# Kernel tuning notes

Hardware: AMD Instinct MI355X
Metric: run time of the kernel (lower is better)

## Reference

```python
import jax, jax.numpy as jnp
import numpy as np
from jax import lax

V, E, H = 32000, 512, 1024  # vocab, embedding_dim, hidden_dim
S, B, T = 50, 64, 10        # src len, batch, max decode steps
SOS = 0


def setup_inputs() -> dict:
    key = jax.random.key(0)
    ks = jax.random.split(key, 16)
    sc = 0.02
    n = jax.random.normal
    return {
        "enc_out": n(ks[0], (S, B, 2 * H), jnp.float32),
        "hidden": n(ks[1], (1, B, H), jnp.float32),
        "target": jax.random.randint(ks[2], (B, T), 0, V),
        "emb": n(ks[3], (V, E), jnp.float32) * sc,
        "w_ih": n(ks[4], (3 * H, E), jnp.float32) * sc,
        "w_hh": n(ks[5], (3 * H, H), jnp.float32) * sc,
        "b_ih": n(ks[6], (3 * H,), jnp.float32) * sc,
        "b_hh": n(ks[7], (3 * H,), jnp.float32) * sc,
        "wa_w": n(ks[8], (H, H), jnp.float32) * sc,
        "wa_b": n(ks[9], (H,), jnp.float32) * sc,
        "ua_w": n(ks[10], (H, 2 * H), jnp.float32) * sc,
        "ua_b": n(ks[11], (H,), jnp.float32) * sc,
        "va_w": n(ks[12], (1, H), jnp.float32) * sc,
        "va_b": n(ks[13], (1,), jnp.float32) * sc,
    }


def reference(enc_out, hidden, target, emb, w_ih, w_hh, b_ih, b_hh,
              wa_w, wa_b, ua_w, ua_b, va_w, va_b):
    b, t = target.shape

    def gru_cell(x, h):
        gi = x @ w_ih.T + b_ih          # [B, 3H]
        gh = h @ w_hh.T + b_hh          # [B, 3H]
        ir, iz, inn = jnp.split(gi, 3, axis=-1)
        hr, hz, hn = jnp.split(gh, 3, axis=-1)
        r = jax.nn.sigmoid(ir + hr)
        z = jax.nn.sigmoid(iz + hz)
        nng = jnp.tanh(inn + r * hn)
        return (1.0 - z) * nng + z * h

    # teacher-forced decoder inputs: [SOS, target[:, :-1]] -> [T, B]
    dec_in = jnp.concatenate(
        [jnp.full((b, 1), SOS, dtype=target.dtype), target[:, : t - 1]], axis=1)
    xs = emb[dec_in].transpose(1, 0, 2)  # [T, B, E] (dropout is identity in eval)

    def step(h, x):
        h2 = gru_cell(x, h)
        return h2, h2

    h_last, hs = lax.scan(step, hidden[0], xs)   # hs: [T, B, H]

    keys = enc_out.transpose(1, 0, 2)            # [B, S, 2H]
    uk = keys @ ua_w.T + ua_b                    # [B, S, H]
    wq = hs @ wa_w.T + wa_b                      # [T, B, H]
    # additive (Bahdanau) scores: [T, B, S]
    scores = (jnp.tanh(wq[:, :, None, :] + uk[None]) @ va_w.T + va_b)[..., 0]
    weights = jax.nn.softmax(scores, axis=-1)    # over source positions
    context = jnp.einsum('tbs,bsd->btd', weights, keys)  # [B, T, 2H]
    out = jax.nn.log_softmax(context, axis=-1)   # [B, T, 2H]
    return out, h_last
```

## Files before the change

### kernel.cpp

```cpp
#include <hip/hip_runtime.h>
#include <math.h>

#define VOCAB 32000
#define E_DIM 512
#define H_DIM 1024
#define S_LEN 50
#define B_SZ 64
#define T_LEN 10
#define H3 (3 * H_DIM)
#define D2H (2 * H_DIM)

typedef __attribute__((ext_vector_type(8))) short short8;
typedef __attribute__((ext_vector_type(4))) float floatx4;

__device__ __forceinline__ ushort f2b(float f) {
    union { float f; uint32_t u; } x; x.f = f;
    uint32_t r = (x.u + 0x7fff + ((x.u >> 16) & 1)) >> 16;
    return (ushort)r;
}
__device__ __forceinline__ float b2f(ushort u) {
    union { float f; uint32_t u; } x; x.u = ((uint32_t)u) << 16;
    return x.f;
}
__device__ __forceinline__ float fast_sigmoid(float x) {
    x = fminf(fmaxf(x, -30.f), 30.f);
    return 1.f / (1.f + __expf(-x));
}
__device__ __forceinline__ float fast_tanh(float x) {
    x = fminf(fmaxf(x, -15.f), 15.f);
    float e = __expf(2.f * x);
    return (e - 1.f) / (e + 1.f);
}

#define PB0 1536
#define PB1 (PB0 + 3072)
#define PB2 (PB1 + 2048)
#define PB3 (PB2 + 1024)
#define PB4 (PB3 + 3200)
#define PB5 (PB4 + 640)
#define PB6 (PB5 + 64)

__device__ __forceinline__ void cvt_chunk(const float* src, ushort* dst, int i) {
    float4 v = ((const float4*)src)[i];
    ushort4 o;
    o.x = f2b(v.x); o.y = f2b(v.y); o.z = f2b(v.z); o.w = f2b(v.w);
    ((ushort4*)dst)[i] = o;
}

__global__ __launch_bounds__(256) void prep(
    const float* __restrict__ w_ih, ushort* __restrict__ w_ihb,
    const float* __restrict__ w_hh, ushort* __restrict__ w_hhb,
    const float* __restrict__ ua_w, ushort* __restrict__ ua_wb,
    const float* __restrict__ wa_w, ushort* __restrict__ wa_wb,
    const float* __restrict__ enc_out, ushort* __restrict__ keysb,
    const int* __restrict__ target, const float* __restrict__ emb,
    ushort* __restrict__ Xb,
    const float* __restrict__ hidden, ushort* __restrict__ hb0,
    int* __restrict__ bar) {
    int bid = blockIdx.x, tid = threadIdx.x;
    if (bid == 0) {
        for (int i = tid; i < 4096; i += 256)
            __hip_atomic_store(&bar[i], 0, __ATOMIC_RELAXED, __HIP_MEMORY_SCOPE_SYSTEM);
    }
    if (bid < PB0) {
        cvt_chunk(w_ih, w_ihb, bid * 256 + tid);
    } else if (bid < PB1) {
        cvt_chunk(w_hh, w_hhb, (bid - PB0) * 256 + tid);
    } else if (bid < PB2) {
        cvt_chunk(ua_w, ua_wb, (bid - PB1) * 256 + tid);
    } else if (bid < PB3) {
        cvt_chunk(wa_w, wa_wb, (bid - PB2) * 256 + tid);
    } else if (bid < PB4) {
        int bs = bid - PB3;
        int b = bs / S_LEN, s = bs % S_LEN;
        const float* src = enc_out + ((size_t)s * B_SZ + b) * D2H;
        ushort* dst = keysb + (size_t)bs * D2H;
#pragma unroll
        for (int p = 0; p < 2; ++p) {
            int i = tid + p * 256;
            float4 v = ((const float4*)src)[i];
            ushort4 o;
            o.x = f2b(v.x); o.y = f2b(v.y); o.z = f2b(v.z); o.w = f2b(v.w);
            ((ushort4*)dst)[i] = o;
        }
    } else if (bid < PB5) {
        int m = bid - PB4;
        int t = m / B_SZ, b = m % B_SZ;
        int idx = (t == 0) ? 0 : target[b * T_LEN + (t - 1)];
        if (tid < 128) {
            const float* src = emb + (size_t)idx * E_DIM;
            float4 v = ((const float4*)src)[tid];
            ushort4 o;
            o.x = f2b(v.x); o.y = f2b(v.y); o.z = f2b(v.z); o.w = f2b(v.w);
            ((ushort4*)(Xb + (size_t)m * E_DIM))[tid] = o;
        }
    } else {
        cvt_chunk(hidden, hb0, (bid - PB5) * 256 + tid);
    }
}

struct GemmArgs {
    const ushort* A; const ushort* W; const float* bias;
    float* Cf; ushort* C16;
    int M, N, K, nbn, nblk;
};

__global__ __launch_bounds__(256) void gemm_bf16(GemmArgs g0, GemmArgs g1) {
    const bool first = (int)blockIdx.x < g0.nblk;
    GemmArgs g = first ? g0 : g1;
    const int bid = first ? blockIdx.x : (blockIdx.x - g0.nblk);

    __shared__ ushort As[64 * 72];
    __shared__ ushort Bs[128 * 72];

    const int tid = threadIdx.x;
    const int w = tid >> 6, lane = tid & 63;
    const int lm = lane & 15, q = lane >> 4;
    const int wm = w >> 1, wn = w & 1;
    const int n0 = (bid % g.nbn) * 128;
    const int m0 = (bid / g.nbn) * 64;
    const int K = g.K;

    floatx4 acc[2][4];
#pragma unroll
    for (int i = 0; i < 2; ++i)
#pragma unroll
        for (int j = 0; j < 4; ++j)
            acc[i][j] = (floatx4){0.f, 0.f, 0.f, 0.f};

    short8 ar[2], br[4];
    auto load_tiles = [&](int k0) {
#pragma unroll
        for (int p = 0; p < 2; ++p) {
            int c = tid + p * 256;
            ar[p] = *(const short8*)&g.A[(size_t)(m0 + (c >> 3)) * K + k0 + (c & 7) * 8];
        }
#pragma unroll
        for (int p = 0; p < 4; ++p) {
            int c = tid + p * 256;
            br[p] = *(const short8*)&g.W[(size_t)(n0 + (c >> 3)) * K + k0 + (c & 7) * 8];
        }
    };

    load_tiles(0);
    for (int k0 = 0; k0 < K; k0 += 64) {
#pragma unroll
        for (int p = 0; p < 2; ++p) {
            int c = tid + p * 256;
            *(short8*)&As[(c >> 3) * 72 + (c & 7) * 8] = ar[p];
        }
#pragma unroll
        for (int p = 0; p < 4; ++p) {
            int c = tid + p * 256;
            *(short8*)&Bs[(c >> 3) * 72 + (c & 7) * 8] = br[p];
        }
        __syncthreads();
        if (k0 + 64 < K) load_tiles(k0 + 64);

#pragma unroll
        for (int kk = 0; kk < 2; ++kk) {
            short8 af[2], bf[4];
#pragma unroll
            for (int i = 0; i < 2; ++i)
                af[i] = *(const short8*)&As[(wm * 32 + i * 16 + lm) * 72 + kk * 32 + q * 8];
#pragma unroll
            for (int j = 0; j < 4; ++j)
                bf[j] = *(const short8*)&Bs[(wn * 64 + j * 16 + lm) * 72 + kk * 32 + q * 8];
#pragma unroll
            for (int i = 0; i < 2; ++i)
#pragma unroll
                for (int j = 0; j < 4; ++j)
                    acc[i][j] = __builtin_amdgcn_mfma_f32_16x16x32_bf16(af[i], bf[j], acc[i][j], 0, 0, 0);
        }
        __syncthreads();
    }

    float bv[4];
#pragma unroll
    for (int j = 0; j < 4; ++j)
        bv[j] = g.bias[n0 + wn * 64 + j * 16 + lm];
#pragma unroll
    for (int i = 0; i < 2; ++i) {
#pragma unroll
        for (int j = 0; j < 4; ++j) {
            int col = n0 + wn * 64 + j * 16 + lm;
#pragma unroll
            for (int r = 0; r < 4; ++r) {
                int row = m0 + wm * 32 + i * 16 + q * 4 + r;
                float v = acc[i][j][r] + bv[j];
                if (g.C16) g.C16[(size_t)row * g.N + col] = f2b(v);
                else       g.Cf[(size_t)row * g.N + col] = v;
            }
        }
    }
}

#define GRU_BLOCKS 64
#define WS_STRIDE 1032

__device__ __forceinline__ void grid_barrier(int* __restrict__ bar, int t, int bid) {
    __syncthreads();
    if (threadIdx.x == 0) {
        int g = bid & 7;
        int sub = __hip_atomic_fetch_add(&bar[(t * 8 + g) * 32], 1,
                                         __ATOMIC_RELAXED, __HIP_MEMORY_SCOPE_SYSTEM);
        if (sub == 7) {
            int m = __hip_atomic_fetch_add(&bar[2560 + t * 32], 1,
                                           __ATOMIC_RELAXED, __HIP_MEMORY_SCOPE_SYSTEM);
            if (m == 7)
                __hip_atomic_store(&bar[3040], t + 1,
                                   __ATOMIC_RELAXED, __HIP_MEMORY_SCOPE_SYSTEM);
        }
        while (__hip_atomic_load(&bar[3040], __ATOMIC_RELAXED,
                                 __HIP_MEMORY_SCOPE_SYSTEM) <= t)
            __builtin_amdgcn_s_sleep(1);
    }
    __syncthreads();
}

__global__ __launch_bounds__(256, 1) void gru_persistent(
    const ushort* __restrict__ w_hhb, const float* __restrict__ bhh,
    const float* __restrict__ GI, const float* __restrict__ hidden,
    const ushort* __restrict__ hb0, ushort* __restrict__ hsb,
    float* __restrict__ outTail, int* __restrict__ bar) {
    __shared__ ushort Ws[48 * WS_STRIDE];
    const int tid = threadIdx.x;
    const int w = tid >> 6, lane = tid & 63;
    const int lm = lane & 15, q = lane >> 4;
    const int bid = blockIdx.x;
    const int j0 = bid * 16;
    const int j = j0 + lm;

#pragma unroll
    for (int p = 0; p < 24; ++p) {
        int c = tid + p * 256;
        int row = c >> 7, off = c & 127;
        int grow = (row >> 4) * H_DIM + j0 + (row & 15);
        *(short8*)&Ws[row * WS_STRIDE + off * 8] =
            *(const short8*)&w_hhb[(size_t)grow * H_DIM + off * 8];
    }

    const float bhr = bhh[j], bhz = bhh[H_DIM + j], bhn = bhh[2 * H_DIM + j];

    float hf[4];
#pragma unroll
    for (int r = 0; r < 4; ++r)
        hf[r] = hidden[(size_t)(w * 16 + q * 4 + r) * H_DIM + j];

    float ir[4], iz[4], inn[4];
#pragma unroll
    for (int r = 0; r < 4; ++r) {
        const float* gi = GI + (size_t)(w * 16 + q * 4 + r) * H3 + j;
        ir[r] = gi[0]; iz[r] = gi[H_DIM]; inn[r] = gi[2 * H_DIM];
    }

    __syncthreads();

    for (int t = 0; t < T_LEN; ++t) {
        const ushort* hin = (t == 0) ? hb0 : hsb + (size_t)(t - 1) * B_SZ * H_DIM;
        ushort* hout = hsb + (size_t)t * B_SZ * H_DIM;
        const ushort* arow = hin + (size_t)(w * 16 + lm) * H_DIM + q * 8;

        short8 hr[32];
        asm volatile(
            "global_load_dwordx4 %[h0], %[a], off sc0 sc1\n\t"
            "global_load_dwordx4 %[h1], %[a], off offset:64 sc0 sc1\n\t"
            "global_load_dwordx4 %[h2], %[a], off offset:128 sc0 sc1\n\t"
            "global_load_dwordx4 %[h3], %[a], off offset:192 sc0 sc1\n\t"
            "global_load_dwordx4 %[h4], %[a], off offset:256 sc0 sc1\n\t"
            "global_load_dwordx4 %[h5], %[a], off offset:320 sc0 sc1\n\t"
            "global_load_dwordx4 %[h6], %[a], off offset:384 sc0 sc1\n\t"
            "global_load_dwordx4 %[h7], %[a], off offset:448 sc0 sc1\n\t"
            "global_load_dwordx4 %[h8], %[a], off offset:512 sc0 sc1\n\t"
            "global_load_dwordx4 %[h9], %[a], off offset:576 sc0 sc1\n\t"
            "global_load_dwordx4 %[h10], %[a], off offset:640 sc0 sc1\n\t"
            "global_load_dwordx4 %[h11], %[a], off offset:704 sc0 sc1\n\t"
            "global_load_dwordx4 %[h12], %[a], off offset:768 sc0 sc1\n\t"
            "global_load_dwordx4 %[h13], %[a], off offset:832 sc0 sc1\n\t"
            "global_load_dwordx4 %[h14], %[a], off offset:896 sc0 sc1\n\t"
            "global_load_dwordx4 %[h15], %[a], off offset:960 sc0 sc1\n\t"
            "global_load_dwordx4 %[h16], %[a], off offset:1024 sc0 sc1\n\t"
            "global_load_dwordx4 %[h17], %[a], off offset:1088 sc0 sc1\n\t"
            "global_load_dwordx4 %[h18], %[a], off offset:1152 sc0 sc1\n\t"
            "global_load_dwordx4 %[h19], %[a], off offset:1216 sc0 sc1\n\t"
            "global_load_dwordx4 %[h20], %[a], off offset:1280 sc0 sc1\n\t"
            "global_load_dwordx4 %[h21], %[a], off offset:1344 sc0 sc1\n\t"
            "global_load_dwordx4 %[h22], %[a], off offset:1408 sc0 sc1\n\t"
            "global_load_dwordx4 %[h23], %[a], off offset:1472 sc0 sc1\n\t"
            "global_load_dwordx4 %[h24], %[a], off offset:1536 sc0 sc1\n\t"
            "global_load_dwordx4 %[h25], %[a], off offset:1600 sc0 sc1\n\t"
            "global_load_dwordx4 %[h26], %[a], off offset:1664 sc0 sc1\n\t"
            "global_load_dwordx4 %[h27], %[a], off offset:1728 sc0 sc1\n\t"
            "global_load_dwordx4 %[h28], %[a], off offset:1792 sc0 sc1\n\t"
            "global_load_dwordx4 %[h29], %[a], off offset:1856 sc0 sc1\n\t"
            "global_load_dwordx4 %[h30], %[a], off offset:1920 sc0 sc1\n\t"
            "global_load_dwordx4 %[h31], %[a], off offset:1984 sc0 sc1\n\t"
            "s_waitcnt vmcnt(0)"
            : [h0] "=&v"(hr[0]), [h1] "=&v"(hr[1]), [h2] "=&v"(hr[2]), [h3] "=&v"(hr[3]),
              [h4] "=&v"(hr[4]), [h5] "=&v"(hr[5]), [h6] "=&v"(hr[6]), [h7] "=&v"(hr[7]),
              [h8] "=&v"(hr[8]), [h9] "=&v"(hr[9]), [h10] "=&v"(hr[10]), [h11] "=&v"(hr[11]),
              [h12] "=&v"(hr[12]), [h13] "=&v"(hr[13]), [h14] "=&v"(hr[14]), [h15] "=&v"(hr[15]),
              [h16] "=&v"(hr[16]), [h17] "=&v"(hr[17]), [h18] "=&v"(hr[18]), [h19] "=&v"(hr[19]),
              [h20] "=&v"(hr[20]), [h21] "=&v"(hr[21]), [h22] "=&v"(hr[22]), [h23] "=&v"(hr[23]),
              [h24] "=&v"(hr[24]), [h25] "=&v"(hr[25]), [h26] "=&v"(hr[26]), [h27] "=&v"(hr[27]),
              [h28] "=&v"(hr[28]), [h29] "=&v"(hr[29]), [h30] "=&v"(hr[30]), [h31] "=&v"(hr[31])
            : [a] "v"(arow)
            : "memory");

        floatx4 accr = {0.f, 0.f, 0.f, 0.f};
        floatx4 accz = {0.f, 0.f, 0.f, 0.f};
        floatx4 accn = {0.f, 0.f, 0.f, 0.f};

#pragma unroll
        for (int it = 0; it < 8; ++it) {
#pragma unroll
            for (int kk = 0; kk < 4; ++kk) {
                const short8 af = hr[it * 4 + kk];
                const int ko = it * 128 + kk * 32 + q * 8;
                short8 b0 = *(const short8*)&Ws[(lm) * WS_STRIDE + ko];
                short8 b1 = *(const short8*)&Ws[(16 + lm) * WS_STRIDE + ko];
                short8 b2 = *(const short8*)&Ws[(32 + lm) * WS_STRIDE + ko];
                accr = __builtin_amdgcn_mfma_f32_16x16x32_bf16(af, b0, accr, 0, 0, 0);
                accz = __builtin_amdgcn_mfma_f32_16x16x32_bf16(af, b1, accz, 0, 0, 0);
                accn = __builtin_amdgcn_mfma_f32_16x16x32_bf16(af, b2, accn, 0, 0, 0);
            }
        }

        int h16v[4];
#pragma unroll
        for (int r = 0; r < 4; ++r) {
            float rg = fast_sigmoid(ir[r] + accr[r] + bhr);
            float z  = fast_sigmoid(iz[r] + accz[r] + bhz);
            float ng = fast_tanh(inn[r] + rg * (accn[r] + bhn));
            float hnew = (1.f - z) * ng + z * hf[r];
            hf[r] = hnew;
            h16v[r] = (int)f2b(hnew);
            if (t == T_LEN - 1) {
                int b = w * 16 + q * 4 + r;
                outTail[(size_t)b * H_DIM + j] = hnew;
            }
        }
#pragma unroll
        for (int r = 0; r < 4; ++r) {
            int pv = __shfl(h16v[r], (lane + 1) & 63);
            if ((lm & 1) == 0) {
                int b = w * 16 + q * 4 + r;
                uint packed = (uint)(h16v[r] & 0xffff) | ((uint)pv << 16);
                __hip_atomic_store((uint*)hout + ((size_t)b * H_DIM + j) / 2, packed,
                                   __ATOMIC_RELAXED, __HIP_MEMORY_SCOPE_SYSTEM);
            }
        }

        if (t < T_LEN - 1) {
#pragma unroll
            for (int r = 0; r < 4; ++r) {
                const float* gi = GI + (size_t)((t + 1) * B_SZ + w * 16 + q * 4 + r) * H3 + j;
                ir[r] = gi[0]; iz[r] = gi[H_DIM]; inn[r] = gi[2 * H_DIM];
            }
            grid_barrier(bar, t, bid);
        }
    }
}

__global__ __launch_bounds__(256) void attn_ctx(
    const ushort* __restrict__ WQ16, const ushort* __restrict__ UK16,
    const float* __restrict__ va_w, const float* __restrict__ va_b,
    const ushort* __restrict__ keysb, float* __restrict__ out) {
    __shared__ float wq_s[H_DIM];
    __shared__ float va_s[H_DIM];
    __shared__ float sc[S_LEN];
    __shared__ float wred[4];
    __shared__ float sred[4];
    const int bt = blockIdx.x;
    const int t = bt >> 6, b = bt & 63;
    const int tid = threadIdx.x;
    const int wave = tid >> 6, lane = tid & 63;

    for (int hh = tid; hh < H_DIM; hh += 256) {
        wq_s[hh] = b2f(WQ16[(size_t)(t * B_SZ + b) * H_DIM + hh]);
        va_s[hh] = va_w[hh];
    }
    __syncthreads();

    for (int s = wave; s < S_LEN; s += 4) {
        const ushort* uk = UK16 + ((size_t)b * S_LEN + s) * H_DIM + lane * 16;
        short8 u0 = *(const short8*)&uk[0];
        short8 u1 = *(const short8*)&uk[8];
        float acc = 0.f;
        const int h0 = lane * 16;
#pragma unroll
        for (int i = 0; i < 8; ++i)
            acc += fast_tanh(wq_s[h0 + i] + b2f((ushort)u0[i])) * va_s[h0 + i];
#pragma unroll
        for (int i = 0; i < 8; ++i)
            acc += fast_tanh(wq_s[h0 + 8 + i] + b2f((ushort)u1[i])) * va_s[h0 + 8 + i];
        for (int off = 32; off > 0; off >>= 1) acc += __shfl_down(acc, off);
        if (lane == 0) sc[s] = acc + va_b[0];
    }
    __syncthreads();

    if (tid < 64) {
        float v = (tid < S_LEN) ? sc[tid] : -INFINITY;
        float m = v;
        for (int off = 32; off > 0; off >>= 1) m = fmaxf(m, __shfl_down(m, off));
        m = __shfl(m, 0);
        float e = (tid < S_LEN) ? __expf(v - m) : 0.f;
        float sum = e;
        for (int off = 32; off > 0; off >>= 1) sum += __shfl_down(sum, off);
        sum = __shfl(sum, 0);
        if (tid < S_LEN) sc[tid] = e / sum;
    }
    __syncthreads();

    float c[8];
#pragma unroll
    for (int i = 0; i < 8; ++i) c[i] = 0.f;
    const ushort* kb = keysb + (size_t)b * S_LEN * D2H + tid * 8;
    for (int s = 0; s < S_LEN; ++s) {
        float ws = sc[s];
        short8 kv = *(const short8*)&kb[(size_t)s * D2H];
#pragma unroll
        for (int i = 0; i < 8; ++i) c[i] += ws * b2f((ushort)kv[i]);
    }

    float m = c[0];
#pragma unroll
    for (int i = 1; i < 8; ++i) m = fmaxf(m, c[i]);
    for (int off = 32; off > 0; off >>= 1) m = fmaxf(m, __shfl_down(m, off));
    if (lane == 0) wred[wave] = m;
    __syncthreads();
    if (tid == 0) wred[0] = fmaxf(fmaxf(wred[0], wred[1]), fmaxf(wred[2], wred[3]));
    __syncthreads();
    m = wred[0];
    float sum = 0.f;
#pragma unroll
    for (int i = 0; i < 8; ++i) sum += __expf(c[i] - m);
    for (int off = 32; off > 0; off >>= 1) sum += __shfl_down(sum, off);
    if (lane == 0) sred[wave] = sum;
    __syncthreads();
    if (tid == 0) sred[0] = sred[0] + sred[1] + sred[2] + sred[3];
    __syncthreads();
    float lse = m + __logf(sred[0]);

    float* o = out + ((size_t)b * T_LEN + t) * D2H + tid * 8;
#pragma unroll
    for (int i = 0; i < 8; ++i) o[i] = c[i] - lse;
}

extern "C" void kernel_launch(void* const* d_in, const int* in_sizes, int n_in,
                              void* d_out, int out_size, void* d_ws, size_t ws_size,
                              hipStream_t stream) {
    const float* enc_out = (const float*)d_in[0];
    const float* hidden  = (const float*)d_in[1];
    const int*   target  = (const int*)d_in[2];
    const float* emb     = (const float*)d_in[3];
    const float* w_ih    = (const float*)d_in[4];
    const float* w_hh    = (const float*)d_in[5];
    const float* b_ih    = (const float*)d_in[6];
    const float* b_hh    = (const float*)d_in[7];
    const float* wa_w    = (const float*)d_in[8];
    const float* wa_b    = (const float*)d_in[9];
    const float* ua_w    = (const float*)d_in[10];
    const float* ua_b    = (const float*)d_in[11];
    const float* va_w    = (const float*)d_in[12];
    const float* va_b    = (const float*)d_in[13];
    float* out = (float*)d_out;

    const int TB = T_LEN * B_SZ;
    const int BS = B_SZ * S_LEN;

    char* p = (char*)d_ws;
    int*    bar   = (int*)p;    p += 4096 * 4;
    float*  GI    = (float*)p;  p += (size_t)TB * H3 * 4;
    p = (char*)(((uintptr_t)p + 255) & ~(uintptr_t)255);
    ushort* keysb = (ushort*)p; p += (size_t)BS * D2H * 2;
    ushort* Xb    = (ushort*)p; p += (size_t)TB * E_DIM * 2;
    ushort* w_ihb = (ushort*)p; p += (size_t)H3 * E_DIM * 2;
    ushort* w_hhb = (ushort*)p; p += (size_t)H3 * H_DIM * 2;
    ushort* ua_wb = (ushort*)p; p += (size_t)H_DIM * D2H * 2;
    ushort* wa_wb = (ushort*)p; p += (size_t)H_DIM * H_DIM * 2;
    ushort* hb0   = (ushort*)p; p += (size_t)B_SZ * H_DIM * 2;
    ushort* hsb   = (ushort*)p; p += (size_t)TB * H_DIM * 2;
    ushort* UK16  = (ushort*)p; p += (size_t)BS * H_DIM * 2;
    ushort* WQ16  = (ushort*)p; p += (size_t)TB * H_DIM * 2;

    prep<<<PB6, 256, 0, stream>>>(w_ih, w_ihb, w_hh, w_hhb, ua_w, ua_wb, wa_w, wa_wb,
                                  enc_out, keysb, target, emb, Xb, hidden, hb0, bar);

    GemmArgs guk = { keysb, ua_wb, ua_b, nullptr, UK16,
                     BS, H_DIM, D2H, H_DIM / 128, (BS / 64) * (H_DIM / 128) };
    GemmArgs ggi = { Xb, w_ihb, b_ih, GI, nullptr,
                     TB, H3, E_DIM, H3 / 128, (TB / 64) * (H3 / 128) };
    gemm_bf16<<<guk.nblk + ggi.nblk, 256, 0, stream>>>(guk, ggi);

    float* outTail = out + (size_t)B_SZ * T_LEN * D2H;
    gru_persistent<<<GRU_BLOCKS, 256, 0, stream>>>(w_hhb, b_hh, GI, hidden,
                                                   hb0, hsb, outTail, bar);

    GemmArgs gwq = { hsb, wa_wb, wa_b, nullptr, WQ16,
                     TB, H_DIM, H_DIM, H_DIM / 128, (TB / 64) * (H_DIM / 128) };
    gemm_bf16<<<gwq.nblk, 256, 0, stream>>>(gwq, gwq);

    attn_ctx<<<B_SZ * T_LEN, 256, 0, stream>>>(WQ16, UK16, va_w, va_b, keysb, out);
}
```

Before: 309.2 us.

## Fuse all stages into one persistent megakernel overlapping GRU with prep and GEMMs

Replaces the five separate launches (prep, input GEMMs, persistent GRU, WQ GEMM, attention) with a single 256-block persistent kernel. 64 blocks run the GRU recurrence while the other 192 blocks convert weights and inputs and compute the GI and UK GEMMs. Per-timestep readiness flags let the GRU start as soon as each step's GI tiles exist, and flag barriers separate the later phases. It also seems to drop the separate bf16 conversion buffer for w_hh. The aim is to remove launch gaps and to hide the serial GRU under the parallel GEMM work, at the cost of spin-wait barriers and a reliance on all 256 blocks being co-resident.

```diff
diff --git a/kernel.cpp b/kernel.cpp
--- a/kernel.cpp
+++ b/kernel.cpp
@@ -10,6 +10,11 @@
 #define H3 (3 * H_DIM)
 #define D2H (2 * H_DIM)
 
+#define NBLK 256
+#define NGRU 64
+#define NGEMM 192
+#define WS_STRIDE 1032
+
 typedef __attribute__((ext_vector_type(8))) short short8;
 typedef __attribute__((ext_vector_type(4))) float floatx4;
 
@@ -32,13 +37,39 @@
     return (e - 1.f) / (e + 1.f);
 }
 
-#define PB0 1536
-#define PB1 (PB0 + 3072)
-#define PB2 (PB1 + 2048)
-#define PB3 (PB2 + 1024)
-#define PB4 (PB3 + 3200)
-#define PB5 (PB4 + 640)
-#define PB6 (PB5 + 64)
+__device__ __forceinline__ int ld_flag(int* p) {
+    return __hip_atomic_load(p, __ATOMIC_RELAXED, __HIP_MEMORY_SCOPE_SYSTEM);
+}
+__device__ __forceinline__ void st_flag(int* p, int v) {
+    __hip_atomic_store(p, v, __ATOMIC_RELAXED, __HIP_MEMORY_SCOPE_SYSTEM);
+}
+
+__device__ void flag_barrier(int* flags, int nf, int self, int val, bool fenced) {
+    __syncthreads();
+    if (threadIdx.x == 0) {
+        if (fenced) __builtin_amdgcn_fence(__ATOMIC_RELEASE, "agent");
+        st_flag(&flags[self * 16], val);
+    }
+    if (threadIdx.x < 64) {
+        for (;;) {
+            bool miss = false;
+            for (int i = threadIdx.x; i < nf; i += 64)
+                if (ld_flag(&flags[i * 16]) < val) miss = true;
+            if (__ballot(miss) == 0ull) break;
+            __builtin_amdgcn_s_sleep(2);
+        }
+    }
+    if (fenced && threadIdx.x == 0)
+        __builtin_amdgcn_fence(__ATOMIC_ACQUIRE, "agent");
+    __syncthreads();
+}
+
+__device__ void wait_flag_ge(int* p, int target) {
+    if (threadIdx.x == 0) {
+        while (ld_flag(p) < target) __builtin_amdgcn_s_sleep(2);
+    }
+    __syncthreads();
+}
 
 __device__ __forceinline__ void cvt_chunk(const float* src, ushort* dst, int i) {
     float4 v = ((const float4*)src)[i];
@@ -47,79 +78,16 @@
     ((ushort4*)dst)[i] = o;
 }
 
-__global__ __launch_bounds__(256) void prep(
-    const float* __restrict__ w_ih, ushort* __restrict__ w_ihb,
-    const float* __restrict__ w_hh, ushort* __restrict__ w_hhb,
-    const float* __restrict__ ua_w, ushort* __restrict__ ua_wb,
-    const float* __restrict__ wa_w, ushort* __restrict__ wa_wb,
-    const float* __restrict__ enc_out, ushort* __restrict__ keysb,
-    const int* __restrict__ target, const float* __restrict__ emb,
-    ushort* __restrict__ Xb,
-    const float* __restrict__ hidden, ushort* __restrict__ hb0,
-    int* __restrict__ bar) {
-    int bid = blockIdx.x, tid = threadIdx.x;
-    if (bid == 0) {
-        for (int i = tid; i < 4096; i += 256)
-            __hip_atomic_store(&bar[i], 0, __ATOMIC_RELAXED, __HIP_MEMORY_SCOPE_SYSTEM);
-    }
-    if (bid < PB0) {
-        cvt_chunk(w_ih, w_ihb, bid * 256 + tid);
-    } else if (bid < PB1) {
-        cvt_chunk(w_hh, w_hhb, (bid - PB0) * 256 + tid);
-    } else if (bid < PB2) {
-        cvt_chunk(ua_w, ua_wb, (bid - PB1) * 256 + tid);
-    } else if (bid < PB3) {
-        cvt_chunk(wa_w, wa_wb, (bid - PB2) * 256 + tid);
-    } else if (bid < PB4) {
-        int bs = bid - PB3;
-        int b = bs / S_LEN, s = bs % S_LEN;
-        const float* src = enc_out + ((size_t)s * B_SZ + b) * D2H;
-        ushort* dst = keysb + (size_t)bs * D2H;
-#pragma unroll
-        for (int p = 0; p < 2; ++p) {
-            int i = tid + p * 256;
-            float4 v = ((const float4*)src)[i];
-            ushort4 o;
-            o.x = f2b(v.x); o.y = f2b(v.y); o.z = f2b(v.z); o.w = f2b(v.w);
-            ((ushort4*)dst)[i] = o;
-        }
-    } else if (bid < PB5) {
-        int m = bid - PB4;
-        int t = m / B_SZ, b = m % B_SZ;
-        int idx = (t == 0) ? 0 : target[b * T_LEN + (t - 1)];
-        if (tid < 128) {
-            const float* src = emb + (size_t)idx * E_DIM;
-            float4 v = ((const float4*)src)[tid];
-            ushort4 o;
-            o.x = f2b(v.x); o.y = f2b(v.y); o.z = f2b(v.z); o.w = f2b(v.w);
-            ((ushort4*)(Xb + (size_t)m * E_DIM))[tid] = o;
-        }
-    } else {
-        cvt_chunk(hidden, hb0, (bid - PB5) * 256 + tid);
-    }
-}
-
-struct GemmArgs {
-    const ushort* A; const ushort* W; const float* bias;
-    float* Cf; ushort* C16;
-    int M, N, K, nbn, nblk;
-};
-
-__global__ __launch_bounds__(256) void gemm_bf16(GemmArgs g0, GemmArgs g1) {
-    const bool first = (int)blockIdx.x < g0.nblk;
-    GemmArgs g = first ? g0 : g1;
-    const int bid = first ? blockIdx.x : (blockIdx.x - g0.nblk);
-
-    __shared__ ushort As[64 * 72];
-    __shared__ ushort Bs[128 * 72];
+__device__ void gemm_tile(const ushort* __restrict__ A, const ushort* __restrict__ W,
+                          const float* __restrict__ bias, float* Cf, ushort* C16,
+                          int N, int K, int m0, int n0, int mode, ushort* SMEM) {
+    ushort* As = SMEM;
+    ushort* Bs = SMEM + 64 * 72;
 
     const int tid = threadIdx.x;
     const int w = tid >> 6, lane = tid & 63;
     const int lm = lane & 15, q = lane >> 4;
     const int wm = w >> 1, wn = w & 1;
-    const int n0 = (bid % g.nbn) * 128;
-    const int m0 = (bid / g.nbn) * 64;
-    const int K = g.K;
 
     floatx4 acc[2][4];
 #pragma unroll
@@ -133,12 +101,12 @@
 #pragma unroll
         for (int p = 0; p < 2; ++p) {
             int c = tid + p * 256;
-            ar[p] = *(const short8*)&g.A[(size_t)(m0 + (c >> 3)) * K + k0 + (c & 7) * 8];
+            ar[p] = *(const short8*)&A[(size_t)(m0 + (c >> 3)) * K + k0 + (c & 7) * 8];
         }
 #pragma unroll
         for (int p = 0; p < 4; ++p) {
             int c = tid + p * 256;
-            br[p] = *(const short8*)&g.W[(size_t)(n0 + (c >> 3)) * K + k0 + (c & 7) * 8];
+            br[p] = *(const short8*)&W[(size_t)(n0 + (c >> 3)) * K + k0 + (c & 7) * 8];
         }
     };
 
@@ -178,7 +146,7 @@
     float bv[4];
 #pragma unroll
     for (int j = 0; j < 4; ++j)
-        bv[j] = g.bias[n0 + wn * 64 + j * 16 + lm];
+        bv[j] = bias[n0 + wn * 64 + j * 16 + lm];
 #pragma unroll
     for (int i = 0; i < 2; ++i) {
 #pragma unroll
@@ -188,190 +156,40 @@
             for (int r = 0; r < 4; ++r) {
                 int row = m0 + wm * 32 + i * 16 + q * 4 + r;
                 float v = acc[i][j][r] + bv[j];
-                if (g.C16) g.C16[(size_t)row * g.N + col] = f2b(v);
-                else       g.Cf[(size_t)row * g.N + col] = v;
-            }
-        }
-    }
-}
-
-#define GRU_BLOCKS 64
-#define WS_STRIDE 1032
-
-__device__ __forceinline__ void grid_barrier(int* __restrict__ bar, int t, int bid) {
-    __syncthreads();
-    if (threadIdx.x == 0) {
-        int g = bid & 7;
-        int sub = __hip_atomic_fetch_add(&bar[(t * 8 + g) * 32], 1,
-                                         __ATOMIC_RELAXED, __HIP_MEMORY_SCOPE_SYSTEM);
-        if (sub == 7) {
-            int m = __hip_atomic_fetch_add(&bar[2560 + t * 32], 1,
+                if (mode == 1) {
+                    C16[(size_t)row * N + col] = f2b(v);
+                } else if (mode == 0) {
+                    float pv = __shfl(v, (lane + 1) & 63);
+                    if ((lm & 1) == 0) {
+                        union { float f[2]; unsigned long long u; } pk;
+                        pk.f[0] = v; pk.f[1] = pv;
+                        __hip_atomic_store((unsigned long long*)&Cf[(size_t)row * N + col],
+                                           pk.u, __ATOMIC_RELAXED, __HIP_MEMORY_SCOPE_SYSTEM);
+                    }
+                } else {
+                    int a16 = (int)f2b(v);
+                    int pv = __shfl(a16, (lane + 1) & 63);
+                    if ((lm & 1) == 0) {
+                        uint packed = (uint)(a16 & 0xffff) | ((uint)pv << 16);
+                        __hip_atomic_store((uint*)(C16 + (size_t)row * N + col), packed,
                                            __ATOMIC_RELAXED, __HIP_MEMORY_SCOPE_SYSTEM);
-            if (m == 7)
-                __hip_atomic_store(&bar[3040], t + 1,
-                                   __ATOMIC_RELAXED, __HIP_MEMORY_SCOPE_SYSTEM);
-        }
-        while (__hip_atomic_load(&bar[3040], __ATOMIC_RELAXED,
-                                 __HIP_MEMORY_SCOPE_SYSTEM) <= t)
-            __builtin_amdgcn_s_sleep(1);
-    }
-    __syncthreads();
-}
-
-__global__ __launch_bounds__(256, 1) void gru_persistent(
-    const ushort* __restrict__ w_hhb, const float* __restrict__ bhh,
-    const float* __restrict__ GI, const float* __restrict__ hidden,
-    const ushort* __restrict__ hb0, ushort* __restrict__ hsb,
-    float* __restrict__ outTail, int* __restrict__ bar) {
-    __shared__ ushort Ws[48 * WS_STRIDE];
-    const int tid = threadIdx.x;
-    const int w = tid >> 6, lane = tid & 63;
-    const int lm = lane & 15, q = lane >> 4;
-    const int bid = blockIdx.x;
-    const int j0 = bid * 16;
-    const int j = j0 + lm;
-
-#pragma unroll
-    for (int p = 0; p < 24; ++p) {
-        int c = tid + p * 256;
-        int row = c >> 7, off = c & 127;
-        int grow = (row >> 4) * H_DIM + j0 + (row & 15);
-        *(short8*)&Ws[row * WS_STRIDE + off * 8] =
-            *(const short8*)&w_hhb[(size_t)grow * H_DIM + off * 8];
-    }
-
-    const float bhr = bhh[j], bhz = bhh[H_DIM + j], bhn = bhh[2 * H_DIM + j];
-
-    float hf[4];
-#pragma unroll
-    for (int r = 0; r < 4; ++r)
-        hf[r] = hidden[(size_t)(w * 16 + q * 4 + r) * H_DIM + j];
-
-    float ir[4], iz[4], inn[4];
-#pragma unroll
-    for (int r = 0; r < 4; ++r) {
-        const float* gi = GI + (size_t)(w * 16 + q * 4 + r) * H3 + j;
-        ir[r] = gi[0]; iz[r] = gi[H_DIM]; inn[r] = gi[2 * H_DIM];
-    }
-
-    __syncthreads();
-
-    for (int t = 0; t < T_LEN; ++t) {
-        const ushort* hin = (t == 0) ? hb0 : hsb + (size_t)(t - 1) * B_SZ * H_DIM;
-        ushort* hout = hsb + (size_t)t * B_SZ * H_DIM;
-        const ushort* arow = hin + (size_t)(w * 16 + lm) * H_DIM + q * 8;
-
-        short8 hr[32];
-        asm volatile(
-            "global_load_dwordx4 %[h0], %[a], off sc0 sc1\n\t"
-            "global_load_dwordx4 %[h1], %[a], off offset:64 sc0 sc1\n\t"
-            "global_load_dwordx4 %[h2], %[a], off offset:128 sc0 sc1\n\t"
-            "global_load_dwordx4 %[h3], %[a], off offset:192 sc0 sc1\n\t"
-            "global_load_dwordx4 %[h4], %[a], off offset:256 sc0 sc1\n\t"
-            "global_load_dwordx4 %[h5], %[a], off offset:320 sc0 sc1\n\t"
-            "global_load_dwordx4 %[h6], %[a], off offset:384 sc0 sc1\n\t"
-            "global_load_dwordx4 %[h7], %[a], off offset:448 sc0 sc1\n\t"
-            "global_load_dwordx4 %[h8], %[a], off offset:512 sc0 sc1\n\t"
-            "global_load_dwordx4 %[h9], %[a], off offset:576 sc0 sc1\n\t"
-            "global_load_dwordx4 %[h10], %[a], off offset:640 sc0 sc1\n\t"
-            "global_load_dwordx4 %[h11], %[a], off offset:704 sc0 sc1\n\t"
-            "global_load_dwordx4 %[h12], %[a], off offset:768 sc0 sc1\n\t"
-            "global_load_dwordx4 %[h13], %[a], off offset:832 sc0 sc1\n\t"
-            "global_load_dwordx4 %[h14], %[a], off offset:896 sc0 sc1\n\t"
-            "global_load_dwordx4 %[h15], %[a], off offset:960 sc0 sc1\n\t"
-            "global_load_dwordx4 %[h16], %[a], off offset:1024 sc0 sc1\n\t"
-            "global_load_dwordx4 %[h17], %[a], off offset:1088 sc0 sc1\n\t"
-            "global_load_dwordx4 %[h18], %[a], off offset:1152 sc0 sc1\n\t"
-            "global_load_dwordx4 %[h19], %[a], off offset:1216 sc0 sc1\n\t"
-            "global_load_dwordx4 %[h20], %[a], off offset:1280 sc0 sc1\n\t"
-            "global_load_dwordx4 %[h21], %[a], off offset:1344 sc0 sc1\n\t"
-            "global_load_dwordx4 %[h22], %[a], off offset:1408 sc0 sc1\n\t"
-            "global_load_dwordx4 %[h23], %[a], off offset:1472 sc0 sc1\n\t"
-            "global_load_dwordx4 %[h24], %[a], off offset:1536 sc0 sc1\n\t"
-            "global_load_dwordx4 %[h25], %[a], off offset:1600 sc0 sc1\n\t"
-            "global_load_dwordx4 %[h26], %[a], off offset:1664 sc0 sc1\n\t"
-            "global_load_dwordx4 %[h27], %[a], off offset:1728 sc0 sc1\n\t"
-            "global_load_dwordx4 %[h28], %[a], off offset:1792 sc0 sc1\n\t"
-            "global_load_dwordx4 %[h29], %[a], off offset:1856 sc0 sc1\n\t"
-            "global_load_dwordx4 %[h30], %[a], off offset:1920 sc0 sc1\n\t"
-            "global_load_dwordx4 %[h31], %[a], off offset:1984 sc0 sc1\n\t"
-            "s_waitcnt vmcnt(0)"
-            : [h0] "=&v"(hr[0]), [h1] "=&v"(hr[1]), [h2] "=&v"(hr[2]), [h3] "=&v"(hr[3]),
-              [h4] "=&v"(hr[4]), [h5] "=&v"(hr[5]), [h6] "=&v"(hr[6]), [h7] "=&v"(hr[7]),
-              [h8] "=&v"(hr[8]), [h9] "=&v"(hr[9]), [h10] "=&v"(hr[10]), [h11] "=&v"(hr[11]),
-              [h12] "=&v"(hr[12]), [h13] "=&v"(hr[13]), [h14] "=&v"(hr[14]), [h15] "=&v"(hr[15]),
-              [h16] "=&v"(hr[16]), [h17] "=&v"(hr[17]), [h18] "=&v"(hr[18]), [h19] "=&v"(hr[19]),
-              [h20] "=&v"(hr[20]), [h21] "=&v"(hr[21]), [h22] "=&v"(hr[22]), [h23] "=&v"(hr[23]),
-              [h24] "=&v"(hr[24]), [h25] "=&v"(hr[25]), [h26] "=&v"(hr[26]), [h27] "=&v"(hr[27]),
-              [h28] "=&v"(hr[28]), [h29] "=&v"(hr[29]), [h30] "=&v"(hr[30]), [h31] "=&v"(hr[31])
-            : [a] "v"(arow)
-            : "memory");
-
-        floatx4 accr = {0.f, 0.f, 0.f, 0.f};
-        floatx4 accz = {0.f, 0.f, 0.f, 0.f};
-        floatx4 accn = {0.f, 0.f, 0.f, 0.f};
-
-#pragma unroll
-        for (int it = 0; it < 8; ++it) {
-#pragma unroll
-            for (int kk = 0; kk < 4; ++kk) {
-                const short8 af = hr[it * 4 + kk];
-                const int ko = it * 128 + kk * 32 + q * 8;
-                short8 b0 = *(const short8*)&Ws[(lm) * WS_STRIDE + ko];
-                short8 b1 = *(const short8*)&Ws[(16 + lm) * WS_STRIDE + ko];
-                short8 b2 = *(const short8*)&Ws[(32 + lm) * WS_STRIDE + ko];
-                accr = __builtin_amdgcn_mfma_f32_16x16x32_bf16(af, b0, accr, 0, 0, 0);
-                accz = __builtin_amdgcn_mfma_f32_16x16x32_bf16(af, b1, accz, 0, 0, 0);
-                accn = __builtin_amdgcn_mfma_f32_16x16x32_bf16(af, b2, accn, 0, 0, 0);
-            }
-        }
-
-        int h16v[4];
-#pragma unroll
-        for (int r = 0; r < 4; ++r) {
-            float rg = fast_sigmoid(ir[r] + accr[r] + bhr);
-            float z  = fast_sigmoid(iz[r] + accz[r] + bhz);
-            float ng = fast_tanh(inn[r] + rg * (accn[r] + bhn));
-            float hnew = (1.f - z) * ng + z * hf[r];
-            hf[r] = hnew;
-            h16v[r] = (int)f2b(hnew);
-            if (t == T_LEN - 1) {
-                int b = w * 16 + q * 4 + r;
-                outTail[(size_t)b * H_DIM + j] = hnew;
-            }
-        }
-#pragma unroll
-        for (int r = 0; r < 4; ++r) {
-            int pv = __shfl(h16v[r], (lane + 1) & 63);
-            if ((lm & 1) == 0) {
-                int b = w * 16 + q * 4 + r;
-                uint packed = (uint)(h16v[r] & 0xffff) | ((uint)pv << 16);
-                __hip_atomic_store((uint*)hout + ((size_t)b * H_DIM + j) / 2, packed,
-                                   __ATOMIC_RELAXED, __HIP_MEMORY_SCOPE_SYSTEM);
-            }
-        }
-
-        if (t < T_LEN - 1) {
-#pragma unroll
-            for (int r = 0; r < 4; ++r) {
-                const float* gi = GI + (size_t)((t + 1) * B_SZ + w * 16 + q * 4 + r) * H3 + j;
-                ir[r] = gi[0]; iz[r] = gi[H_DIM]; inn[r] = gi[2 * H_DIM];
-            }
-            grid_barrier(bar, t, bid);
-        }
-    }
-}
-
-__global__ __launch_bounds__(256) void attn_ctx(
-    const ushort* __restrict__ WQ16, const ushort* __restrict__ UK16,
-    const float* __restrict__ va_w, const float* __restrict__ va_b,
-    const ushort* __restrict__ keysb, float* __restrict__ out) {
-    __shared__ float wq_s[H_DIM];
-    __shared__ float va_s[H_DIM];
-    __shared__ float sc[S_LEN];
-    __shared__ float wred[4];
-    __shared__ float sred[4];
-    const int bt = blockIdx.x;
+                    }
+                }
+            }
+        }
+    }
+}
+
+__device__ void attn_unit(int bt, const ushort* __restrict__ WQ16,
+                          const ushort* __restrict__ UK16,
+                          const float* __restrict__ va_w, const float* __restrict__ va_b,
+                          const ushort* __restrict__ keysb, float* __restrict__ out,
+                          ushort* SMEM) {
+    float* wq_s = (float*)SMEM;
+    float* va_s = wq_s + 1024;
+    float* scb  = va_s + 1024;
+    float* wred = scb + 64;
+    float* sred = wred + 4;
     const int t = bt >> 6, b = bt & 63;
     const int tid = threadIdx.x;
     const int wave = tid >> 6, lane = tid & 63;
@@ -395,12 +213,12 @@
         for (int i = 0; i < 8; ++i)
             acc += fast_tanh(wq_s[h0 + 8 + i] + b2f((ushort)u1[i])) * va_s[h0 + 8 + i];
         for (int off = 32; off > 0; off >>= 1) acc += __shfl_down(acc, off);
-        if (lane == 0) sc[s] = acc + va_b[0];
+        if (lane == 0) scb[s] = acc + va_b[0];
     }
     __syncthreads();
 
     if (tid < 64) {
-        float v = (tid < S_LEN) ? sc[tid] : -INFINITY;
+        float v = (tid < S_LEN) ? scb[tid] : -INFINITY;
         float m = v;
         for (int off = 32; off > 0; off >>= 1) m = fmaxf(m, __shfl_down(m, off));
         m = __shfl(m, 0);
@@ -408,7 +226,7 @@
         float sum = e;
         for (int off = 32; off > 0; off >>= 1) sum += __shfl_down(sum, off);
         sum = __shfl(sum, 0);
-        if (tid < S_LEN) sc[tid] = e / sum;
+        if (tid < S_LEN) scb[tid] = e / sum;
     }
     __syncthreads();
 
@@ -417,7 +235,7 @@
     for (int i = 0; i < 8; ++i) c[i] = 0.f;
     const ushort* kb = keysb + (size_t)b * S_LEN * D2H + tid * 8;
     for (int s = 0; s < S_LEN; ++s) {
-        float ws = sc[s];
+        float ws = scb[s];
         short8 kv = *(const short8*)&kb[(size_t)s * D2H];
 #pragma unroll
         for (int i = 0; i < 8; ++i) c[i] += ws * b2f((ushort)kv[i]);
@@ -445,6 +263,254 @@
     float* o = out + ((size_t)b * T_LEN + t) * D2H + tid * 8;
 #pragma unroll
     for (int i = 0; i < 8; ++i) o[i] = c[i] - lse;
+    __syncthreads();
+}
+
+__global__ __launch_bounds__(256, 1) void mega(
+    const float* __restrict__ enc_out, const float* __restrict__ hidden,
+    const int* __restrict__ target, const float* __restrict__ emb,
+    const float* __restrict__ w_ih, const float* __restrict__ w_hh,
+    const float* __restrict__ b_ih, const float* __restrict__ b_hh,
+    const float* __restrict__ wa_w, const float* __restrict__ wa_b,
+    const float* __restrict__ ua_w, const float* __restrict__ ua_b,
+    const float* __restrict__ va_w, const float* __restrict__ va_b,
+    float* __restrict__ out,
+    int* __restrict__ bar, float* __restrict__ GI,
+    ushort* __restrict__ keysb, ushort* __restrict__ Xb,
+    ushort* __restrict__ w_ihb, ushort* __restrict__ ua_wb,
+    ushort* __restrict__ wa_wb, ushort* __restrict__ hb0,
+    ushort* __restrict__ hsb, ushort* __restrict__ UK16,
+    ushort* __restrict__ WQ16) {
+    __shared__ ushort SMEM[48 * WS_STRIDE];
+    const int bid = blockIdx.x, tid = threadIdx.x;
+    int* gruF = bar;
+    int* b1F  = bar + 1024;
+    int* b2F  = bar + 4096;
+    int* b3F  = bar + 8192;
+    int* giR  = bar + 12288;
+
+    if (bid < NGRU) {
+        const int w = tid >> 6, lane = tid & 63;
+        const int lm = lane & 15, q = lane >> 4;
+        const int j0 = bid * 16;
+        const int j = j0 + lm;
+
+#pragma unroll
+        for (int p = 0; p < 24; ++p) {
+            int c = tid + p * 256;
+            int row = c >> 7, off = c & 127;
+            int grow = (row >> 4) * H_DIM + j0 + (row & 15);
+            const float* src = &w_hh[(size_t)grow * H_DIM + off * 8];
+            float4 a = ((const float4*)src)[0];
+            float4 bq = ((const float4*)src)[1];
+            short8 s;
+            s[0] = (short)f2b(a.x);  s[1] = (short)f2b(a.y);
+            s[2] = (short)f2b(a.z);  s[3] = (short)f2b(a.w);
+            s[4] = (short)f2b(bq.x); s[5] = (short)f2b(bq.y);
+            s[6] = (short)f2b(bq.z); s[7] = (short)f2b(bq.w);
+            *(short8*)&SMEM[row * WS_STRIDE + off * 8] = s;
+        }
+
+        {
+            int i = bid * 256 + tid;
+            float4 v = ((const float4*)hidden)[i];
+            union { ushort4 s; unsigned long long u; } pk;
+            pk.s.x = f2b(v.x); pk.s.y = f2b(v.y); pk.s.z = f2b(v.z); pk.s.w = f2b(v.w);
+            __hip_atomic_store((unsigned long long*)hb0 + i, pk.u,
+                               __ATOMIC_RELAXED, __HIP_MEMORY_SCOPE_SYSTEM);
+        }
+
+        const float bhr = b_hh[j], bhz = b_hh[H_DIM + j], bhn = b_hh[2 * H_DIM + j];
+        float hf[4];
+#pragma unroll
+        for (int r = 0; r < 4; ++r)
+            hf[r] = hidden[(size_t)(w * 16 + q * 4 + r) * H_DIM + j];
+
+        flag_barrier(gruF, NGRU, bid, 1, false);
+
+        wait_flag_ge(&giR[0], 24);
+
+        float ir[4], iz[4], inn[4];
+#pragma unroll
+        for (int r = 0; r < 4; ++r) {
+            const float* gi = GI + (size_t)(w * 16 + q * 4 + r) * H3 + j;
+            ir[r] = gi[0]; iz[r] = gi[H_DIM]; inn[r] = gi[2 * H_DIM];
+        }
+
+        float* outTail = out + (size_t)B_SZ * T_LEN * D2H;
+
+        for (int t = 0; t < T_LEN; ++t) {
+            const ushort* hin = (t == 0) ? hb0 : hsb + (size_t)(t - 1) * B_SZ * H_DIM;
+            ushort* hout = hsb + (size_t)t * B_SZ * H_DIM;
+            const ushort* arow = hin + (size_t)(w * 16 + lm) * H_DIM + q * 8;
+
+            short8 hr[32];
+            asm volatile(
+                "global_load_dwordx4 %[h0], %[a], off sc0 sc1\n\t"
+                "global_load_dwordx4 %[h1], %[a], off offset:64 sc0 sc1\n\t"
+                "global_load_dwordx4 %[h2], %[a], off offset:128 sc0 sc1\n\t"
+                "global_load_dwordx4 %[h3], %[a], off offset:192 sc0 sc1\n\t"
+                "global_load_dwordx4 %[h4], %[a], off offset:256 sc0 sc1\n\t"
+                "global_load_dwordx4 %[h5], %[a], off offset:320 sc0 sc1\n\t"
+                "global_load_dwordx4 %[h6], %[a], off offset:384 sc0 sc1\n\t"
+                "global_load_dwordx4 %[h7], %[a], off offset:448 sc0 sc1\n\t"
+                "global_load_dwordx4 %[h8], %[a], off offset:512 sc0 sc1\n\t"
+                "global_load_dwordx4 %[h9], %[a], off offset:576 sc0 sc1\n\t"
+                "global_load_dwordx4 %[h10], %[a], off offset:640 sc0 sc1\n\t"
+                "global_load_dwordx4 %[h11], %[a], off offset:704 sc0 sc1\n\t"
+                "global_load_dwordx4 %[h12], %[a], off offset:768 sc0 sc1\n\t"
+                "global_load_dwordx4 %[h13], %[a], off offset:832 sc0 sc1\n\t"
+                "global_load_dwordx4 %[h14], %[a], off offset:896 sc0 sc1\n\t"
+                "global_load_dwordx4 %[h15], %[a], off offset:960 sc0 sc1\n\t"
+                "global_load_dwordx4 %[h16], %[a], off offset:1024 sc0 sc1\n\t"
+                "global_load_dwordx4 %[h17], %[a], off offset:1088 sc0 sc1\n\t"
+                "global_load_dwordx4 %[h18], %[a], off offset:1152 sc0 sc1\n\t"
+                "global_load_dwordx4 %[h19], %[a], off offset:1216 sc0 sc1\n\t"
+                "global_load_dwordx4 %[h20], %[a], off offset:1280 sc0 sc1\n\t"
+                "global_load_dwordx4 %[h21], %[a], off offset:1344 sc0 sc1\n\t"
+                "global_load_dwordx4 %[h22], %[a], off offset:1408 sc0 sc1\n\t"
+                "global_load_dwordx4 %[h23], %[a], off offset:1472 sc0 sc1\n\t"
+                "global_load_dwordx4 %[h24], %[a], off offset:1536 sc0 sc1\n\t"
+                "global_load_dwordx4 %[h25], %[a], off offset:1600 sc0 sc1\n\t"
+                "global_load_dwordx4 %[h26], %[a], off offset:1664 sc0 sc1\n\t"
+                "global_load_dwordx4 %[h27], %[a], off offset:1728 sc0 sc1\n\t"
+                "global_load_dwordx4 %[h28], %[a], off offset:1792 sc0 sc1\n\t"
+                "global_load_dwordx4 %[h29], %[a], off offset:1856 sc0 sc1\n\t"
+                "global_load_dwordx4 %[h30], %[a], off offset:1920 sc0 sc1\n\t"
+                "global_load_dwordx4 %[h31], %[a], off offset:1984 sc0 sc1\n\t"
+                "s_waitcnt vmcnt(0)"
+                : [h0] "=&v"(hr[0]), [h1] "=&v"(hr[1]), [h2] "=&v"(hr[2]), [h3] "=&v"(hr[3]),
+                  [h4] "=&v"(hr[4]), [h5] "=&v"(hr[5]), [h6] "=&v"(hr[6]), [h7] "=&v"(hr[7]),
+                  [h8] "=&v"(hr[8]), [h9] "=&v"(hr[9]), [h10] "=&v"(hr[10]), [h11] "=&v"(hr[11]),
+                  [h12] "=&v"(hr[12]), [h13] "=&v"(hr[13]), [h14] "=&v"(hr[14]), [h15] "=&v"(hr[15]),
+                  [h16] "=&v"(hr[16]), [h17] "=&v"(hr[17]), [h18] "=&v"(hr[18]), [h19] "=&v"(hr[19]),
+                  [h20] "=&v"(hr[20]), [h21] "=&v"(hr[21]), [h22] "=&v"(hr[22]), [h23] "=&v"(hr[23]),
+                  [h24] "=&v"(hr[24]), [h25] "=&v"(hr[25]), [h26] "=&v"(hr[26]), [h27] "=&v"(hr[27]),
+                  [h28] "=&v"(hr[28]), [h29] "=&v"(hr[29]), [h30] "=&v"(hr[30]), [h31] "=&v"(hr[31])
+                : [a] "v"(arow)
+                : "memory");
+
+            floatx4 accr = {0.f, 0.f, 0.f, 0.f};
+            floatx4 accz = {0.f, 0.f, 0.f, 0.f};
+            floatx4 accn = {0.f, 0.f, 0.f, 0.f};
+
+#pragma unroll
+            for (int it = 0; it < 8; ++it) {
+#pragma unroll
+                for (int kk = 0; kk < 4; ++kk) {
+                    const short8 af = hr[it * 4 + kk];
+                    const int ko = it * 128 + kk * 32 + q * 8;
+                    short8 b0 = *(const short8*)&SMEM[(lm) * WS_STRIDE + ko];
+                    short8 b1 = *(const short8*)&SMEM[(16 + lm) * WS_STRIDE + ko];
+                    short8 b2 = *(const short8*)&SMEM[(32 + lm) * WS_STRIDE + ko];
+                    accr = __builtin_amdgcn_mfma_f32_16x16x32_bf16(af, b0, accr, 0, 0, 0);
+                    accz = __builtin_amdgcn_mfma_f32_16x16x32_bf16(af, b1, accz, 0, 0, 0);
+                    accn = __builtin_amdgcn_mfma_f32_16x16x32_bf16(af, b2, accn, 0, 0, 0);
+                }
+            }
+
+            int h16v[4];
+#pragma unroll
+            for (int r = 0; r < 4; ++r) {
+                float rg = fast_sigmoid(ir[r] + accr[r] + bhr);
+                float z  = fast_sigmoid(iz[r] + accz[r] + bhz);
+                float ng = fast_tanh(inn[r] + rg * (accn[r] + bhn));
+                float hnew = (1.f - z) * ng + z * hf[r];
+                hf[r] = hnew;
+                h16v[r] = (int)f2b(hnew);
+                if (t == T_LEN - 1) {
+                    int b = w * 16 + q * 4 + r;
+                    outTail[(size_t)b * H_DIM + j] = hnew;
+                }
+            }
+#pragma unroll
+            for (int r = 0; r < 4; ++r) {
+                int pv = __shfl(h16v[r], (lane + 1) & 63);
+                if ((lm & 1) == 0) {
+                    int b = w * 16 + q * 4 + r;
+                    uint packed = (uint)(h16v[r] & 0xffff) | ((uint)pv << 16);
+                    __hip_atomic_store((uint*)hout + ((size_t)b * H_DIM + j) / 2, packed,
+                                       __ATOMIC_RELAXED, __HIP_MEMORY_SCOPE_SYSTEM);
+                }
+            }
+
+            if (t < T_LEN - 1) {
+                wait_flag_ge(&giR[(t + 1) * 16], 24);
+#pragma unroll
+                for (int r = 0; r < 4; ++r) {
+                    const float* gi = GI + (size_t)((t + 1) * B_SZ + w * 16 + q * 4 + r) * H3 + j;
+                    ir[r] = gi[0]; iz[r] = gi[H_DIM]; inn[r] = gi[2 * H_DIM];
+                }
+                flag_barrier(gruF, NGRU, bid, t + 2, false);
+            }
+        }
+    } else {
+        const int g = bid - NGRU;
+        if (g == 0 && tid < 10) st_flag(&giR[tid * 16], 0);
+
+        for (int u = g * 44; u < g * 44 + 44; ++u) {
+            if (u < 1536) {
+                cvt_chunk(w_ih, w_ihb, u * 256 + tid);
+            } else if (u < 3584) {
+                cvt_chunk(ua_w, ua_wb, (u - 1536) * 256 + tid);
+            } else if (u < 4608) {
+                cvt_chunk(wa_w, wa_wb, (u - 3584) * 256 + tid);
+            } else if (u < 7808) {
+                int bs = u - 4608;
+                int b = bs / S_LEN, s = bs % S_LEN;
+                const float* src = enc_out + ((size_t)s * B_SZ + b) * D2H;
+                ushort* dst = keysb + (size_t)bs * D2H;
+#pragma unroll
+                for (int p = 0; p < 2; ++p) {
+                    int i = tid + p * 256;
+                    float4 v = ((const float4*)src)[i];
+                    ushort4 o;
+                    o.x = f2b(v.x); o.y = f2b(v.y); o.z = f2b(v.z); o.w = f2b(v.w);
+                    ((ushort4*)dst)[i] = o;
+                }
+            } else {
+                int m = u - 7808;
+                int t = m / B_SZ, b = m % B_SZ;
+                int idx = (t == 0) ? 0 : target[b * T_LEN + (t - 1)];
+                if (tid < 128) {
+                    const float* src = emb + (size_t)idx * E_DIM;
+                    float4 v = ((const float4*)src)[tid];
+                    ushort4 o;
+                    o.x = f2b(v.x); o.y = f2b(v.y); o.z = f2b(v.z); o.w = f2b(v.w);
+                    ((ushort4*)(Xb + (size_t)m * E_DIM))[tid] = o;
+                }
+            }
+        }
+
+        flag_barrier(b1F, NGEMM, g, 1, true);
+
+        for (int tile = g; tile < 640; tile += NGEMM) {
+            if (tile < 240) {
+                int t = tile / 24, nn = tile % 24;
+                gemm_tile(Xb, w_ihb, b_ih, GI, nullptr, H3, E_DIM,
+                          t * 64, nn * 128, 0, SMEM);
+                __syncthreads();
+                if (tid == 0)
+                    __hip_atomic_fetch_add(&giR[t * 16], 1,
+                                           __ATOMIC_RELAXED, __HIP_MEMORY_SCOPE_SYSTEM);
+            } else {
+                int u = tile - 240;
+                gemm_tile(keysb, ua_wb, ua_b, nullptr, UK16, H_DIM, D2H,
+                          (u / 8) * 64, (u % 8) * 128, 1, SMEM);
+            }
+        }
+    }
+
+    flag_barrier(b2F, NBLK, bid, 1, true);
+
+    if (bid < 80) {
+        gemm_tile(hsb, wa_wb, wa_b, nullptr, WQ16, H_DIM, H_DIM,
+                  (bid / 8) * 64, (bid % 8) * 128, 2, SMEM);
+    }
+    flag_barrier(b3F, NBLK, bid, 1, false);
+
+    for (int u = bid; u < 640; u += NBLK)
+        attn_unit(u, WQ16, UK16, va_w, va_b, keysb, out, SMEM);
 }
 
 extern "C" void kernel_launch(void* const* d_in, const int* in_sizes, int n_in,
@@ -470,13 +536,12 @@
     const int BS = B_SZ * S_LEN;
 
     char* p = (char*)d_ws;
-    int*    bar   = (int*)p;    p += 4096 * 4;
+    int*    bar   = (int*)p;    p += 16384 * 4;
     float*  GI    = (float*)p;  p += (size_t)TB * H3 * 4;
     p = (char*)(((uintptr_t)p + 255) & ~(uintptr_t)255);
     ushort* keysb = (ushort*)p; p += (size_t)BS * D2H * 2;
     ushort* Xb    = (ushort*)p; p += (size_t)TB * E_DIM * 2;
     ushort* w_ihb = (ushort*)p; p += (size_t)H3 * E_DIM * 2;
-    ushort* w_hhb = (ushort*)p; p += (size_t)H3 * H_DIM * 2;
     ushort* ua_wb = (ushort*)p; p += (size_t)H_DIM * D2H * 2;
     ushort* wa_wb = (ushort*)p; p += (size_t)H_DIM * H_DIM * 2;
     ushort* hb0   = (ushort*)p; p += (size_t)B_SZ * H_DIM * 2;
@@ -484,22 +549,8 @@
     ushort* UK16  = (ushort*)p; p += (size_t)BS * H_DIM * 2;
     ushort* WQ16  = (ushort*)p; p += (size_t)TB * H_DIM * 2;
 
-    prep<<<PB6, 256, 0, stream>>>(w_ih, w_ihb, w_hh, w_hhb, ua_w, ua_wb, wa_w, wa_wb,
-                                  enc_out, keysb, target, emb, Xb, hidden, hb0, bar);
-
-    GemmArgs guk = { keysb, ua_wb, ua_b, nullptr, UK16,
-                     BS, H_DIM, D2H, H_DIM / 128, (BS / 64) * (H_DIM / 128) };
-    GemmArgs ggi = { Xb, w_ihb, b_ih, GI, nullptr,
-                     TB, H3, E_DIM, H3 / 128, (TB / 64) * (H3 / 128) };
-    gemm_bf16<<<guk.nblk + ggi.nblk, 256, 0, stream>>>(guk, ggi);
-
-    float* outTail = out + (size_t)B_SZ * T_LEN * D2H;
-    gru_persistent<<<GRU_BLOCKS, 256, 0, stream>>>(w_hhb, b_hh, GI, hidden,
-                                                   hb0, hsb, outTail, bar);
-
-    GemmArgs gwq = { hsb, wa_wb, wa_b, nullptr, WQ16,
-                     TB, H_DIM, H_DIM, H_DIM / 128, (TB / 64) * (H_DIM / 128) };
-    gemm_bf16<<<gwq.nblk, 256, 0, stream>>>(gwq, gwq);
-
-    attn_ctx<<<B_SZ * T_LEN, 256, 0, stream>>>(WQ16, UK16, va_w, va_b, keysb, out);
-}
+    mega<<<NBLK, 256, 0, stream>>>(enc_out, hidden, target, emb, w_ih, w_hh,
+                                   b_ih, b_hh, wa_w, wa_b, ua_w, ua_b, va_w, va_b,
+                                   out, bar, GI, keysb, Xb, w_ihb, ua_wb, wa_wb,
+                                   hb0, hsb, UK16, WQ16);
+}
```

After: 345.7 us. 1.12x slower.
